# Performance work log

Hardware: AMD Instinct MI355X
Metric: run time of the kernel (lower is better)

The kernel has to match this reference:

```python
import jax, jax.numpy as jnp
import numpy as np

B, N, C, H, W = 2, 2048, 1024, 16, 8  # batch, seq, dim, heads, band half-width
HD = C // H
SCALE = HD ** -0.5


def band_mask(n, w):
    # rows i: allowed cols lo..hi inclusive, matching get_attn_mask
    i = jnp.arange(n)[:, None]
    j = jnp.arange(n)[None, :]
    lo = jnp.where(i <= w, 0, i - w)
    hi = jnp.where(n - i <= w, n - 1, i + w)
    return (j >= lo) & (j <= hi)  # [N, N] bool


def setup_inputs() -> dict:
    key = jax.random.key(0)
    k1, k2, k3 = jax.random.split(key, 3)
    x = jax.random.normal(k1, (B, N, C), dtype=jnp.float32)
    Wqkv = jax.random.normal(k2, (C, 3 * C), dtype=jnp.float32) * (C ** -0.5)
    Wproj = jax.random.normal(k3, (C, C), dtype=jnp.float32) * (C ** -0.5)
    bproj = jnp.zeros((C,), dtype=jnp.float32)
    return {"x": x, "Wqkv": Wqkv, "Wproj": Wproj, "bproj": bproj}


def reference(x, Wqkv, Wproj, bproj):
    b, n, c = x.shape
    qkv = (x @ Wqkv).reshape(b, n, 3, H, HD)
    qkv = jnp.transpose(qkv, (2, 0, 3, 1, 4))  # [3, B, H, N, HD]
    q, k, v = qkv[0], qkv[1], qkv[2]
    attn = jnp.einsum('bhqd,bhkd->bhqk', q, k) * SCALE
    mask = band_mask(n, W)  # [N, N]
    attn = jnp.where(mask[None, None], attn, jnp.float32(-1e9))
    attn = jax.nn.softmax(attn, axis=-1)
    # dropout omitted (eval mode / deterministic reference)
    out = jnp.einsum('bhqk,bhkd->bhqd', attn, v)
    out = jnp.transpose(out, (0, 2, 1, 3)).reshape(b, n, c)
    return out @ Wproj + bproj
```

## Files before the change

### kernel.cpp

```cpp
#include <hip/hip_runtime.h>

typedef unsigned short ushort_t;
typedef unsigned int uint32;

typedef __bf16 bf16x8 __attribute__((ext_vector_type(8)));
typedef float f32x4 __attribute__((ext_vector_type(4)));

__device__ __forceinline__ uint32 f2bf1(float f) {
  uint32 b = __float_as_uint(f);
  return (b + 0x7FFFu + ((b >> 16) & 1u)) >> 16;
}
__device__ __forceinline__ uint32 packbf2(float a, float b) {
  return f2bf1(a) | (f2bf1(b) << 16);
}
__device__ __forceinline__ float bflo(uint32 u) { return __uint_as_float(u << 16); }
__device__ __forceinline__ float bfhi(uint32 u) { return __uint_as_float(u & 0xFFFF0000u); }

__device__ __forceinline__ void gload16(const void* g, void* l) {
  __builtin_amdgcn_global_load_lds(
      (const __attribute__((address_space(1))) unsigned int*)g,
      (__attribute__((address_space(3))) unsigned int*)l, 16, 0, 0);
}

__global__ __launch_bounds__(256) void cvt_f32_bf16(
    const float* __restrict__ in, ushort_t* __restrict__ out, int n4) {
  int i = blockIdx.x * 256 + threadIdx.x;
  if (i < n4) {
    float4 v = ((const float4*)in)[i];
    uint2 r;
    r.x = packbf2(v.x, v.y);
    r.y = packbf2(v.z, v.w);
    ((uint2*)out)[i] = r;
  }
}

__global__ __launch_bounds__(256) void transpose_cvt(
    const float* __restrict__ Wsrc, ushort_t* __restrict__ Wt, int R, int Cc) {
  __shared__ float tile[32][33];
  const int tx = threadIdx.x & 31, ty = threadIdx.x >> 5;
  const int c0 = blockIdx.x << 5, r0 = blockIdx.y << 5;
#pragma unroll
  for (int i = 0; i < 4; ++i)
    tile[ty + i * 8][tx] = Wsrc[(size_t)(r0 + ty + i * 8) * Cc + c0 + tx];
  __syncthreads();
#pragma unroll
  for (int i = 0; i < 4; ++i)
    Wt[(size_t)(c0 + ty + i * 8) * R + r0 + tx] = (ushort_t)f2bf1(tile[tx][ty + i * 8]);
}

template <bool OUT_BF16>
__global__ __launch_bounds__(256) void gemm_bt(
    const ushort_t* __restrict__ A, const ushort_t* __restrict__ Bt,
    void* __restrict__ Cout, const float* __restrict__ bias,
    const int M, const int Nn, const int K) {
  __shared__ ushort_t lA[128 * 32];
  __shared__ ushort_t lB[128 * 32];
  const int tid = threadIdx.x;
  const int lane = tid & 63, wave = tid >> 6;
  const int wm = wave >> 1, wn = wave & 1;
  const int bm = blockIdx.y << 7, bn = blockIdx.x << 7;

  f32x4 acc[4][4] = {};

  const int srow = tid >> 2, schk = tid & 3;
  const ushort_t* gA = A + (size_t)(bm + srow) * K + schk * 8;
  const ushort_t* gB = Bt + (size_t)(bn + srow) * K + schk * 8;
  ushort_t* lA0 = lA + wave * 512;
  ushort_t* lB0 = lB + wave * 512;

  const int la_off = ((wm << 6) + (lane & 15)) * 32 + ((lane >> 4) << 3);
  const int lb_off = ((wn << 6) + (lane & 15)) * 32 + ((lane >> 4) << 3);

  for (int k0 = 0; k0 < K; k0 += 32) {
    gload16(gA + k0, lA0);
    gload16(gA + k0 + 64 * K, lA0 + 2048);
    gload16(gB + k0, lB0);
    gload16(gB + k0 + 64 * K, lB0 + 2048);
    __syncthreads();
    bf16x8 a[4], b[4];
#pragma unroll
    for (int m = 0; m < 4; ++m) a[m] = *(const bf16x8*)&lA[la_off + m * 512];
#pragma unroll
    for (int n = 0; n < 4; ++n) b[n] = *(const bf16x8*)&lB[lb_off + n * 512];
#pragma unroll
    for (int m = 0; m < 4; ++m)
#pragma unroll
      for (int n = 0; n < 4; ++n)
        acc[m][n] = __builtin_amdgcn_mfma_f32_16x16x32_bf16(a[m], b[n], acc[m][n], 0, 0, 0);
    __syncthreads();
  }

  const int r0 = bm + (wm << 6) + ((lane >> 4) << 2);
  const int c0 = bn + (wn << 6) + (lane & 15);
#pragma unroll
  for (int m = 0; m < 4; ++m)
#pragma unroll
    for (int n = 0; n < 4; ++n)
#pragma unroll
      for (int j = 0; j < 4; ++j) {
        const int row = r0 + m * 16 + j;
        const int col = c0 + n * 16;
        if (OUT_BF16)
          ((ushort_t*)Cout)[(size_t)row * Nn + col] = (ushort_t)f2bf1(acc[m][n][j]);
        else
          ((float*)Cout)[(size_t)row * Nn + col] = acc[m][n][j] + bias[col];
      }
}

__global__ __launch_bounds__(256) void attn_band(
    const ushort_t* __restrict__ qkv, ushort_t* __restrict__ aout) {
  __shared__ float Ks[80 * 68];
  __shared__ float Vs[80 * 68];
  const int tid = threadIdx.x;
  const int i0 = blockIdx.x << 6;
  const int h = blockIdx.y;
  const int b = blockIdx.z;
  const size_t rowbase = (size_t)b * 2048;

  for (int idx = tid; idx < 1280; idx += 256) {
    const int t = idx >> 4, c = idx & 15;
    const int j = i0 - 8 + t;
    float k0 = 0.f, k1 = 0.f, k2 = 0.f, k3 = 0.f;
    float v0 = 0.f, v1 = 0.f, v2 = 0.f, v3 = 0.f;
    if ((unsigned)j < 2048u) {
      const ushort_t* p = qkv + (rowbase + j) * 3072 + (h << 6) + (c << 2);
      uint2 rk = *(const uint2*)(p + 1024);
      uint2 rv = *(const uint2*)(p + 2048);
      k0 = bflo(rk.x); k1 = bfhi(rk.x); k2 = bflo(rk.y); k3 = bfhi(rk.y);
      v0 = bflo(rv.x); v1 = bfhi(rv.x); v2 = bflo(rv.y); v3 = bfhi(rv.y);
    }
    *(float4*)&Ks[t * 68 + (c << 2)] = make_float4(k0, k1, k2, k3);
    *(float4*)&Vs[t * 68 + (c << 2)] = make_float4(v0, v1, v2, v3);
  }
  __syncthreads();

  const int lane = tid & 63, wv = tid >> 6;
  const int qs = lane >> 2, dg = lane & 3;
  const int qi = (wv << 4) + qs;
  const int i = i0 + qi;

  const ushort_t* qp = qkv + (rowbase + i) * 3072 + (h << 6) + (dg << 4);
  float q[16];
  {
    uint4 u0 = *(const uint4*)qp;
    uint4 u1 = *(const uint4*)(qp + 8);
    q[0] = bflo(u0.x); q[1] = bfhi(u0.x); q[2] = bflo(u0.y); q[3] = bfhi(u0.y);
    q[4] = bflo(u0.z); q[5] = bfhi(u0.z); q[6] = bflo(u0.w); q[7] = bfhi(u0.w);
    q[8] = bflo(u1.x); q[9] = bfhi(u1.x); q[10] = bflo(u1.y); q[11] = bfhi(u1.y);
    q[12] = bflo(u1.z); q[13] = bfhi(u1.z); q[14] = bflo(u1.w); q[15] = bfhi(u1.w);
  }

  float s[17];
#pragma unroll
  for (int jo = 0; jo < 17; ++jo) {
    const float* kr = &Ks[(qi + jo) * 68 + (dg << 4)];
    float d = 0.f;
#pragma unroll
    for (int c = 0; c < 4; ++c) {
      float4 kv = *(const float4*)(kr + (c << 2));
      d += q[c * 4 + 0] * kv.x + q[c * 4 + 1] * kv.y +
           q[c * 4 + 2] * kv.z + q[c * 4 + 3] * kv.w;
    }
    d += __shfl_xor(d, 1);
    d += __shfl_xor(d, 2);
    const int jg = i - 8 + jo;
    s[jo] = ((unsigned)jg < 2048u) ? d * 0.125f : -1e30f;
  }
  float m = s[0];
#pragma unroll
  for (int jo = 1; jo < 17; ++jo) m = fmaxf(m, s[jo]);
  float sum = 0.f;
#pragma unroll
  for (int jo = 0; jo < 17; ++jo) {
    s[jo] = __expf(s[jo] - m);
    sum += s[jo];
  }
  const float inv = 1.f / sum;

  float o[16];
#pragma unroll
  for (int dd = 0; dd < 16; ++dd) o[dd] = 0.f;
#pragma unroll
  for (int jo = 0; jo < 17; ++jo) {
    const float* vr = &Vs[(qi + jo) * 68 + (dg << 4)];
    const float w = s[jo];
#pragma unroll
    for (int c = 0; c < 4; ++c) {
      float4 vv = *(const float4*)(vr + (c << 2));
      o[c * 4 + 0] += w * vv.x; o[c * 4 + 1] += w * vv.y;
      o[c * 4 + 2] += w * vv.z; o[c * 4 + 3] += w * vv.w;
    }
  }

  ushort_t* op = aout + (rowbase + i) * 1024 + (h << 6) + (dg << 4);
  uint4 w0, w1;
  w0.x = packbf2(o[0] * inv, o[1] * inv);
  w0.y = packbf2(o[2] * inv, o[3] * inv);
  w0.z = packbf2(o[4] * inv, o[5] * inv);
  w0.w = packbf2(o[6] * inv, o[7] * inv);
  w1.x = packbf2(o[8] * inv, o[9] * inv);
  w1.y = packbf2(o[10] * inv, o[11] * inv);
  w1.z = packbf2(o[12] * inv, o[13] * inv);
  w1.w = packbf2(o[14] * inv, o[15] * inv);
  *(uint4*)op = w0;
  *(uint4*)(op + 8) = w1;
}

extern "C" void kernel_launch(void* const* d_in, const int* in_sizes, int n_in,
                              void* d_out, int out_size, void* d_ws, size_t ws_size,
                              hipStream_t stream) {
  const float* x = (const float*)d_in[0];
  const float* Wqkv = (const float*)d_in[1];
  const float* Wproj = (const float*)d_in[2];
  const float* bproj = (const float*)d_in[3];
  float* out = (float*)d_out;

  char* ws = (char*)d_ws;
  ushort_t* xb    = (ushort_t*)(ws);
  ushort_t* wqkvT = (ushort_t*)(ws + (8u << 20));
  ushort_t* wprT  = (ushort_t*)(ws + (14u << 20));
  ushort_t* qkv   = (ushort_t*)(ws + (16u << 20));
  ushort_t* aoutb = (ushort_t*)(ws + (40u << 20));

  cvt_f32_bf16<<<4096, 256, 0, stream>>>(x, xb, 1048576);
  transpose_cvt<<<dim3(96, 32), 256, 0, stream>>>(Wqkv, wqkvT, 1024, 3072);
  transpose_cvt<<<dim3(32, 32), 256, 0, stream>>>(Wproj, wprT, 1024, 1024);
  gemm_bt<true><<<dim3(24, 32), 256, 0, stream>>>(xb, wqkvT, qkv, nullptr, 4096, 3072, 1024);
  attn_band<<<dim3(32, 16, 2), 256, 0, stream>>>(qkv, aoutb);
  gemm_bt<false><<<dim3(8, 32), 256, 0, stream>>>(aoutb, wprT, out, bproj, 4096, 1024, 1024);
}
```

Measured before the change: 96.22 us.

## Replace QKV GEMM with 256x256 tile, 8-wave pipelined double-buffered kernel

The QKV projection GEMM moves to a new kernel using 256x256 output tiles, 512 threads and a 64-wide K step. Global-to-LDS loads are double-buffered and interleaved with MFMA quadrants, using explicit vmcnt waits, barriers and setprio. The LDS layout is XOR-swizzled to avoid bank conflicts, and workgroups are remapped across XCDs. The aim is to hide memory latency and raise MFMA utilisation, in exchange for far more complex barrier and waitcnt logic that could be fragile, and a 192-workgroup grid that may leave some CUs idle.

```diff
diff --git a/kernel.cpp b/kernel.cpp
--- a/kernel.cpp
+++ b/kernel.cpp
@@ -5,6 +5,9 @@
 
 typedef __bf16 bf16x8 __attribute__((ext_vector_type(8)));
 typedef float f32x4 __attribute__((ext_vector_type(4)));
+
+#define BAR() asm volatile("s_barrier" ::: "memory")
+#define VMCNT(n) asm volatile("s_waitcnt vmcnt(" #n ")" ::: "memory")
 
 __device__ __forceinline__ uint32 f2bf1(float f) {
   uint32 b = __float_as_uint(f);
@@ -46,6 +49,140 @@
 #pragma unroll
   for (int i = 0; i < 4; ++i)
     Wt[(size_t)(c0 + ty + i * 8) * R + r0 + tx] = (ushort_t)f2bf1(tile[tx][ty + i * 8]);
+}
+
+
+__device__ __forceinline__ void stage_half(ushort_t* ldsr, const ushort_t* g,
+                                           int ldK, int tid) {
+  const int r = tid >> 3, s = tid & 7;
+  const int c = ((s ^ (r & 7)) << 3);
+  const int wvb = (tid >> 6) << 9;
+  gload16(g + (size_t)r * ldK + c, ldsr + wvb);
+  gload16(g + (size_t)(r + 64) * ldK + c, ldsr + 4096 + wvb);
+}
+
+#define READ_A(qm_)                                             \
+  {                                                             \
+    const int ab = pA + (qm_) * 4096;                           \
+    a_k0[0] = *(const bf16x8*)&lds[ab + cK0];                   \
+    a_k1[0] = *(const bf16x8*)&lds[ab + cK1];                   \
+    a_k0[1] = *(const bf16x8*)&lds[ab + 1024 + cK0];            \
+    a_k1[1] = *(const bf16x8*)&lds[ab + 1024 + cK1];            \
+    a_k0[2] = *(const bf16x8*)&lds[ab + 2048 + cK0];            \
+    a_k1[2] = *(const bf16x8*)&lds[ab + 2048 + cK1];            \
+    a_k0[3] = *(const bf16x8*)&lds[ab + 3072 + cK0];            \
+    a_k1[3] = *(const bf16x8*)&lds[ab + 3072 + cK1];            \
+  }
+
+#define READ_B(bk0, bk1, qn_)                                   \
+  {                                                             \
+    const int bb = pB + (qn_) * 2048;                           \
+    bk0[0] = *(const bf16x8*)&lds[bb + cK0];                    \
+    bk1[0] = *(const bf16x8*)&lds[bb + cK1];                    \
+    bk0[1] = *(const bf16x8*)&lds[bb + 1024 + cK0];             \
+    bk1[1] = *(const bf16x8*)&lds[bb + 1024 + cK1];             \
+  }
+
+#define MFMAQ(qm_, qn_, bk0, bk1)                                              \
+  {                                                                            \
+    _Pragma("unroll") for (int m = 0; m < 4; ++m) {                            \
+      acc[(qm_) * 4 + m][(qn_) * 2 + 0] = __builtin_amdgcn_mfma_f32_16x16x32_bf16( \
+          a_k0[m], bk0[0], acc[(qm_) * 4 + m][(qn_) * 2 + 0], 0, 0, 0);        \
+      acc[(qm_) * 4 + m][(qn_) * 2 + 0] = __builtin_amdgcn_mfma_f32_16x16x32_bf16( \
+          a_k1[m], bk1[0], acc[(qm_) * 4 + m][(qn_) * 2 + 0], 0, 0, 0);        \
+      acc[(qm_) * 4 + m][(qn_) * 2 + 1] = __builtin_amdgcn_mfma_f32_16x16x32_bf16( \
+          a_k0[m], bk0[1], acc[(qm_) * 4 + m][(qn_) * 2 + 1], 0, 0, 0);        \
+      acc[(qm_) * 4 + m][(qn_) * 2 + 1] = __builtin_amdgcn_mfma_f32_16x16x32_bf16( \
+          a_k1[m], bk1[1], acc[(qm_) * 4 + m][(qn_) * 2 + 1], 0, 0, 0);        \
+    }                                                                          \
+  }
+
+__global__ __launch_bounds__(512, 2) void gemm8p_bt(
+    const ushort_t* __restrict__ A, const ushort_t* __restrict__ Bt,
+    ushort_t* __restrict__ C, const int M, const int Nn, const int K) {
+  __shared__ ushort_t lds[65536];
+  const int tid = threadIdx.x;
+  const int lane = tid & 63, wave = tid >> 6;
+  const int wm = wave >> 2, wn = wave & 3;
+
+  const int q8 = gridDim.x >> 3;
+  const int wg = (blockIdx.x & 7) * q8 + (blockIdx.x >> 3);
+  const int nbn = Nn >> 8;
+  const int bm = (wg / nbn) << 8;
+  const int bn = (wg % nbn) << 8;
+  const int nt = K >> 6;
+
+  const int l15 = lane & 15, l16 = lane >> 4, l7 = l15 & 7;
+  const int cK0 = ((l16 ^ l7) << 3);
+  const int cK1 = (((4 + l16) ^ l7) << 3);
+
+  f32x4 acc[8][4] = {};
+  bf16x8 a_k0[4], a_k1[4], b0_k0[2], b0_k1[2], b1_k0[2], b1_k1[2];
+
+  stage_half(&lds[0], A + (size_t)bm * K, K, tid);
+  stage_half(&lds[8192], A + (size_t)(bm + 128) * K, K, tid);
+  stage_half(&lds[16384], Bt + (size_t)bn * K, K, tid);
+  stage_half(&lds[16384 + 8192], Bt + (size_t)(bn + 128) * K, K, tid);
+  stage_half(&lds[32768 + 16384], Bt + (size_t)bn * K + 64, K, tid);
+  stage_half(&lds[32768 + 16384 + 8192], Bt + (size_t)(bn + 128) * K + 64, K, tid);
+  VMCNT(4);
+  BAR();
+
+  for (int U = 0; U < nt; ++U) {
+    const int p = U & 1;
+    const int pA = p * 32768 + wm * 8192 + l15 * 64;
+    const int pB = p * 32768 + 16384 + (wn >> 1) * 8192 + ((wn & 1) * 64 + l15) * 64;
+    const bool sA = (U + 1) < nt;
+    const bool sB = (U + 2) < nt;
+
+    READ_A(0);
+    READ_B(b0_k0, b0_k1, 0);
+    if (sA) stage_half(&lds[(p ^ 1) * 32768], A + (size_t)bm * K + (U + 1) * 64, K, tid);
+    BAR();
+    __builtin_amdgcn_s_setprio(1);
+    MFMAQ(0, 0, b0_k0, b0_k1);
+    __builtin_amdgcn_s_setprio(0);
+    BAR();
+
+    READ_B(b1_k0, b1_k1, 1);
+    if (sA) stage_half(&lds[(p ^ 1) * 32768 + 8192], A + (size_t)(bm + 128) * K + (U + 1) * 64, K, tid);
+    BAR();
+    __builtin_amdgcn_s_setprio(1);
+    MFMAQ(0, 1, b1_k0, b1_k1);
+    __builtin_amdgcn_s_setprio(0);
+    BAR();
+
+    READ_A(1);
+    if (sB) stage_half(&lds[p * 32768 + 16384], Bt + (size_t)bn * K + (U + 2) * 64, K, tid);
+    BAR();
+    __builtin_amdgcn_s_setprio(1);
+    MFMAQ(1, 1, b1_k0, b1_k1);
+    __builtin_amdgcn_s_setprio(0);
+    BAR();
+
+    if (sB) stage_half(&lds[p * 32768 + 16384 + 8192], Bt + (size_t)(bn + 128) * K + (U + 2) * 64, K, tid);
+    BAR();
+    __builtin_amdgcn_s_setprio(1);
+    MFMAQ(1, 0, b0_k0, b0_k1);
+    __builtin_amdgcn_s_setprio(0);
+    if (sB) {
+      VMCNT(4);
+    } else {
+      VMCNT(0);
+    }
+    BAR();
+  }
+
+  const int crow0 = bm + wm * 128 + (l16 << 2);
+  const int ccol0 = bn + wn * 64 + l15;
+#pragma unroll
+  for (int m = 0; m < 8; ++m)
+#pragma unroll
+    for (int n = 0; n < 4; ++n)
+#pragma unroll
+      for (int j = 0; j < 4; ++j)
+        C[(size_t)(crow0 + m * 16 + j) * Nn + ccol0 + n * 16] =
+            (ushort_t)f2bf1(acc[m][n][j]);
 }
 
 template <bool OUT_BF16>
@@ -225,7 +362,7 @@
   cvt_f32_bf16<<<4096, 256, 0, stream>>>(x, xb, 1048576);
   transpose_cvt<<<dim3(96, 32), 256, 0, stream>>>(Wqkv, wqkvT, 1024, 3072);
   transpose_cvt<<<dim3(32, 32), 256, 0, stream>>>(Wproj, wprT, 1024, 1024);
-  gemm_bt<true><<<dim3(24, 32), 256, 0, stream>>>(xb, wqkvT, qkv, nullptr, 4096, 3072, 1024);
+  gemm8p_bt<<<192, 512, 0, stream>>>(xb, wqkvT, qkv, 4096, 3072, 1024);
   attn_band<<<dim3(32, 16, 2), 256, 0, stream>>>(qkv, aoutb);
   gemm_bt<false><<<dim3(8, 32), 256, 0, stream>>>(aoutb, wprT, out, bproj, 4096, 1024, 1024);
 }
```

Result: faster. 94.21 us (-2.1%).

## Double-buffer GEMM LDS with swizzle, fuse prep kernels, retile projection GEMM

Applied to the files above, without the earlier changes.

Merges the x conversion and both weight transposes into one launch, removing two kernel launches. The GEMM now double-buffers its LDS tiles so the next K-slice's global-to-LDS loads overlap the current MFMAs, and it XOR-swizzles LDS columns to reduce bank conflicts. The output projection GEMM uses 64x128 tiles, doubling its block count so more CUs are busy. The cost is twice the LDS per block, which can lower occupancy.

```diff
diff --git a/kernel.cpp b/kernel.cpp
--- a/kernel.cpp
+++ b/kernel.cpp
@@ -22,80 +22,106 @@
       (__attribute__((address_space(3))) unsigned int*)l, 16, 0, 0);
 }
 
-__global__ __launch_bounds__(256) void cvt_f32_bf16(
-    const float* __restrict__ in, ushort_t* __restrict__ out, int n4) {
-  int i = blockIdx.x * 256 + threadIdx.x;
-  if (i < n4) {
-    float4 v = ((const float4*)in)[i];
+__global__ __launch_bounds__(256) void prep_inputs(
+    const float* __restrict__ x, ushort_t* __restrict__ xb,
+    const float* __restrict__ Wqkv, ushort_t* __restrict__ wqkvT,
+    const float* __restrict__ Wproj, ushort_t* __restrict__ wprT) {
+  int bx = blockIdx.x;
+  const int tid = threadIdx.x;
+  if (bx < 4096) {
+    const int i = bx * 256 + tid;
+    float4 v = ((const float4*)x)[i];
     uint2 r;
     r.x = packbf2(v.x, v.y);
     r.y = packbf2(v.z, v.w);
-    ((uint2*)out)[i] = r;
-  }
-}
-
-__global__ __launch_bounds__(256) void transpose_cvt(
-    const float* __restrict__ Wsrc, ushort_t* __restrict__ Wt, int R, int Cc) {
+    ((uint2*)xb)[i] = r;
+    return;
+  }
+  bx -= 4096;
+  const int gx = bx & 127, gy = bx >> 7;
   __shared__ float tile[32][33];
-  const int tx = threadIdx.x & 31, ty = threadIdx.x >> 5;
-  const int c0 = blockIdx.x << 5, r0 = blockIdx.y << 5;
+  const int tx = tid & 31, ty = tid >> 5;
+  const float* src;
+  ushort_t* dst;
+  int Cc, c0;
+  if (gx < 96) { src = Wqkv;  dst = wqkvT; Cc = 3072; c0 = gx << 5; }
+  else         { src = Wproj; dst = wprT;  Cc = 1024; c0 = (gx - 96) << 5; }
+  const int r0 = gy << 5;
 #pragma unroll
   for (int i = 0; i < 4; ++i)
-    tile[ty + i * 8][tx] = Wsrc[(size_t)(r0 + ty + i * 8) * Cc + c0 + tx];
+    tile[ty + i * 8][tx] = src[(size_t)(r0 + ty + i * 8) * Cc + c0 + tx];
   __syncthreads();
 #pragma unroll
   for (int i = 0; i < 4; ++i)
-    Wt[(size_t)(c0 + ty + i * 8) * R + r0 + tx] = (ushort_t)f2bf1(tile[tx][ty + i * 8]);
-}
-
-template <bool OUT_BF16>
-__global__ __launch_bounds__(256) void gemm_bt(
+    dst[(size_t)(c0 + ty + i * 8) * 1024 + r0 + tx] = (ushort_t)f2bf1(tile[tx][ty + i * 8]);
+}
+
+
+template <int ROWS>
+__device__ __forceinline__ void stage2(ushort_t* dst, const ushort_t* gbase,
+                                       int ldK, int tid) {
+  const int r = tid >> 2, s = tid & 3;
+  const int c = ((s ^ ((r >> 1) & 3)) << 3);
+  const int wvb = (tid >> 6) << 9;
+  const ushort_t* g = gbase + (size_t)r * ldK + c;
+  gload16(g, dst + wvb);
+  if (ROWS == 128) gload16(g + (size_t)64 * ldK, dst + 2048 + wvb);
+}
+
+template <bool OUT_BF16, int MF, int NF>
+__global__ __launch_bounds__(256) void gemm2p(
     const ushort_t* __restrict__ A, const ushort_t* __restrict__ Bt,
     void* __restrict__ Cout, const float* __restrict__ bias,
     const int M, const int Nn, const int K) {
-  __shared__ ushort_t lA[128 * 32];
-  __shared__ ushort_t lB[128 * 32];
+  constexpr int BM = MF * 32, BN = NF * 32;
+  constexpr int AL = BM * 32, BL = BN * 32;
+  __shared__ ushort_t lA[2 * AL];
+  __shared__ ushort_t lB[2 * BL];
   const int tid = threadIdx.x;
   const int lane = tid & 63, wave = tid >> 6;
   const int wm = wave >> 1, wn = wave & 1;
-  const int bm = blockIdx.y << 7, bn = blockIdx.x << 7;
-
-  f32x4 acc[4][4] = {};
-
-  const int srow = tid >> 2, schk = tid & 3;
-  const ushort_t* gA = A + (size_t)(bm + srow) * K + schk * 8;
-  const ushort_t* gB = Bt + (size_t)(bn + srow) * K + schk * 8;
-  ushort_t* lA0 = lA + wave * 512;
-  ushort_t* lB0 = lB + wave * 512;
-
-  const int la_off = ((wm << 6) + (lane & 15)) * 32 + ((lane >> 4) << 3);
-  const int lb_off = ((wn << 6) + (lane & 15)) * 32 + ((lane >> 4) << 3);
-
+  const int bm = blockIdx.y * BM, bn = blockIdx.x * BN;
+
+  const int l15 = lane & 15, l16 = lane >> 4;
+  const int cK = ((l16 ^ ((l15 >> 1) & 3)) << 3);
+
+  const ushort_t* gA = A + (size_t)bm * K;
+  const ushort_t* gB = Bt + (size_t)bn * K;
+
+  f32x4 acc[MF][NF] = {};
+
+  stage2<BM>(lA, gA, K, tid);
+  stage2<BN>(lB, gB, K, tid);
+  __syncthreads();
+
+  int buf = 0;
   for (int k0 = 0; k0 < K; k0 += 32) {
-    gload16(gA + k0, lA0);
-    gload16(gA + k0 + 64 * K, lA0 + 2048);
-    gload16(gB + k0, lB0);
-    gload16(gB + k0 + 64 * K, lB0 + 2048);
-    __syncthreads();
-    bf16x8 a[4], b[4];
-#pragma unroll
-    for (int m = 0; m < 4; ++m) a[m] = *(const bf16x8*)&lA[la_off + m * 512];
-#pragma unroll
-    for (int n = 0; n < 4; ++n) b[n] = *(const bf16x8*)&lB[lb_off + n * 512];
-#pragma unroll
-    for (int m = 0; m < 4; ++m)
-#pragma unroll
-      for (int n = 0; n < 4; ++n)
+    if (k0 + 32 < K) {
+      stage2<BM>(lA + (buf ^ 1) * AL, gA + k0 + 32, K, tid);
+      stage2<BN>(lB + (buf ^ 1) * BL, gB + k0 + 32, K, tid);
+    }
+    bf16x8 a[MF], b[NF];
+#pragma unroll
+    for (int m = 0; m < MF; ++m)
+      a[m] = *(const bf16x8*)&lA[buf * AL + ((wm * MF + m) * 16 + l15) * 32 + cK];
+#pragma unroll
+    for (int n = 0; n < NF; ++n)
+      b[n] = *(const bf16x8*)&lB[buf * BL + ((wn * NF + n) * 16 + l15) * 32 + cK];
+#pragma unroll
+    for (int m = 0; m < MF; ++m)
+#pragma unroll
+      for (int n = 0; n < NF; ++n)
         acc[m][n] = __builtin_amdgcn_mfma_f32_16x16x32_bf16(a[m], b[n], acc[m][n], 0, 0, 0);
     __syncthreads();
-  }
-
-  const int r0 = bm + (wm << 6) + ((lane >> 4) << 2);
-  const int c0 = bn + (wn << 6) + (lane & 15);
-#pragma unroll
-  for (int m = 0; m < 4; ++m)
-#pragma unroll
-    for (int n = 0; n < 4; ++n)
+    buf ^= 1;
+  }
+
+  const int r0 = bm + wm * (MF * 16) + (l16 << 2);
+  const int c0 = bn + wn * (NF * 16) + l15;
+#pragma unroll
+  for (int m = 0; m < MF; ++m)
+#pragma unroll
+    for (int n = 0; n < NF; ++n)
 #pragma unroll
       for (int j = 0; j < 4; ++j) {
         const int row = r0 + m * 16 + j;
@@ -222,10 +248,10 @@
   ushort_t* qkv   = (ushort_t*)(ws + (16u << 20));
   ushort_t* aoutb = (ushort_t*)(ws + (40u << 20));
 
-  cvt_f32_bf16<<<4096, 256, 0, stream>>>(x, xb, 1048576);
-  transpose_cvt<<<dim3(96, 32), 256, 0, stream>>>(Wqkv, wqkvT, 1024, 3072);
-  transpose_cvt<<<dim3(32, 32), 256, 0, stream>>>(Wproj, wprT, 1024, 1024);
-  gemm_bt<true><<<dim3(24, 32), 256, 0, stream>>>(xb, wqkvT, qkv, nullptr, 4096, 3072, 1024);
+  prep_inputs<<<8192, 256, 0, stream>>>(x, xb, Wqkv, wqkvT, Wproj, wprT);
+  gemm2p<true, 4, 4><<<dim3(24, 32), 256, 0, stream>>>(
+      xb, wqkvT, qkv, nullptr, 4096, 3072, 1024);
   attn_band<<<dim3(32, 16, 2), 256, 0, stream>>>(qkv, aoutb);
-  gemm_bt<false><<<dim3(8, 32), 256, 0, stream>>>(aoutb, wprT, out, bproj, 4096, 1024, 1024);
-}
+  gemm2p<false, 2, 4><<<dim3(8, 64), 256, 0, stream>>>(
+      aoutb, wprT, out, bproj, 4096, 1024, 1024);
+}
```

Measured after the change: 82.31 us. 1.17x faster.
